# Optimization experiments

Hardware: AMD Instinct MI355X
Metric: run time of the kernel (lower is better)

Reference implementation:

```python
import jax, jax.numpy as jnp
import numpy as np

N_NODES, N_EDGES, B, K, D = 200000, 500000, 8192, 32, 128
E_DIM, E_EMB, N_CLASS = 128, 128, 60


def setup_inputs() -> dict:
    key = jax.random.key(0)
    ks = jax.random.split(key, 16)
    s = lambda k, shape, scale=0.05: jax.random.normal(k, shape, dtype=jnp.float32) * scale
    return {
        'memory_emb': s(ks[0], (N_NODES, D), 1.0),
        'edge_feat': s(ks[1], (N_EDGES, E_DIM), 1.0),
        'W_q': s(ks[2], (D, D)),
        'W_k': s(ks[3], (D, D)),
        'a': s(ks[4], (2 * D,)),
        'We_w': s(ks[5], (E_DIM, E_EMB)),
        'We_b': s(ks[6], (E_EMB,)),
        'Wuc': s(ks[7], (D + 2 * D + E_EMB, D)),
        'Wc1': s(ks[8], (D, 128)),
        'Wc2': s(ks[9], (128, N_CLASS)),
        'src_idxs': jax.random.randint(ks[10], (B,), 0, N_NODES),
        'dst_idxs': jax.random.randint(ks[11], (B,), 0, N_NODES),
        'edge_idxs': jax.random.randint(ks[12], (B,), 0, N_EDGES),
        'src_neighbors': jax.random.randint(ks[13], (B, K), 0, N_NODES),
        'dst_neighbors': jax.random.randint(ks[14], (B, K), 0, N_NODES),
    }


def reference(memory_emb, edge_feat, W_q, W_k, a, We_w, We_b, Wuc, Wc1, Wc2,
              src_idxs, dst_idxs, edge_idxs, src_neighbors, dst_neighbors):
    def attend(idxs, nbrs):
        self_emb = memory_emb[idxs]                      # [B, D] gather
        nb = memory_emb[nbrs]                            # [B, K, D] gather
        q = self_emb @ W_q                               # [B, D]
        k = jnp.einsum('bkd,de->bke', nb, W_k)           # [B, K, D]
        # GAT-style score: leaky_relu(a . [q || k])
        sq = q @ a[:D]                                   # [B]
        sk = jnp.einsum('bkd,d->bk', k, a[D:])           # [B, K]
        score = jax.nn.leaky_relu(sq[:, None] + sk, 0.2)
        attn = jax.nn.softmax(score, axis=-1)            # [B, K]
        agg = jnp.einsum('bk,bkd->bd', attn, k)          # [B, D]
        return self_emb, agg

    src_e, src_h = attend(src_idxs, src_neighbors)
    dst_e, dst_h = attend(dst_idxs, dst_neighbors)
    e = edge_feat[edge_idxs] @ We_w + We_b               # edge embedding [B, E_EMB]
    msg_src = jax.nn.relu(jnp.concatenate([src_e, src_h, dst_h, e], -1) @ Wuc)
    msg_dst = jax.nn.relu(jnp.concatenate([dst_e, dst_h, src_h, e], -1) @ Wuc)
    logits_src = jax.nn.relu(msg_src @ Wc1) @ Wc2
    logits_dst = jax.nn.relu(msg_dst @ Wc1) @ Wc2
    return jnp.stack([logits_src, logits_dst])           # [2, B, N_CLASS]
```

## Files before the change

### kernel.cpp

```cpp
#include <hip/hip_runtime.h>

#define D 128
#define KNBR 32
#define BATCH 8192
#define NCLASS 60

__global__ __launch_bounds__(256) void k_prep(const float* __restrict__ Wq,
                                              const float* __restrict__ Wk,
                                              const float* __restrict__ a,
                                              float* __restrict__ wqa,
                                              float* __restrict__ wka) {
    int tid = threadIdx.x;
    int i = tid & 127;
    const float* W  = (tid < 128) ? Wq : Wk;
    const float* av = (tid < 128) ? a  : a + D;
    float s = 0.f;
    for (int j = 0; j < D; ++j) s += W[i * D + j] * av[j];
    if (tid < 128) wqa[i] = s; else wka[i] = s;
}

__global__ __launch_bounds__(256) void k_attend(
    const float* __restrict__ mem, const float* __restrict__ Wk,
    const float* __restrict__ wqa, const float* __restrict__ wka,
    const int* __restrict__ src_idxs, const int* __restrict__ dst_idxs,
    const int* __restrict__ src_nb, const int* __restrict__ dst_nb,
    float* __restrict__ selfbuf, float* __restrict__ hbuf)
{
    int b = blockIdx.x;
    int side = blockIdx.y;
    const int* idxs = side ? dst_idxs : src_idxs;
    const int* nbrs = side ? dst_nb  : src_nb;
    int tid = threadIdx.x;

    __shared__ float s_self[D];
    __shared__ float s_wqa[D];
    __shared__ float s_wka[D];
    __shared__ float s_nb[KNBR][D];
    __shared__ int   s_idx[KNBR];
    __shared__ float s_red[D];
    __shared__ float s_skp[KNBR][8];
    __shared__ float s_attn[KNBR];
    __shared__ float s_nbsum[D];
    __shared__ float s_part[2][D];

    int node = idxs[b];
    if (tid < D) { s_self[tid] = mem[(size_t)node * D + tid]; s_wqa[tid] = wqa[tid]; }
    else         { s_wka[tid - D] = wka[tid - D]; }
    if (tid < KNBR) s_idx[tid] = nbrs[b * KNBR + tid];
    __syncthreads();

    {
        int row = tid >> 7;
        int col = tid & 127;
        for (int r = 0; r < KNBR; r += 2) {
            int nn = s_idx[r + row];
            s_nb[r + row][col] = mem[(size_t)nn * D + col];
        }
    }
    if (tid < D) s_red[tid] = s_self[tid] * s_wqa[tid];
    __syncthreads();
    for (int s = 64; s > 0; s >>= 1) {
        if (tid < s) s_red[tid] += s_red[tid + s];
        __syncthreads();
    }
    {
        int k = tid >> 3;
        int p = tid & 7;
        float acc = 0.f;
        int c0 = p * 16;
        #pragma unroll
        for (int c = 0; c < 16; ++c) acc += s_nb[k][c0 + c] * s_wka[c0 + c];
        s_skp[k][p] = acc;
    }
    __syncthreads();
    if (tid < KNBR) {
        float sk = 0.f;
        #pragma unroll
        for (int p = 0; p < 8; ++p) sk += s_skp[tid][p];
        float x = s_red[0] + sk;
        s_attn[tid] = (x >= 0.f) ? x : 0.2f * x;
    }
    __syncthreads();
    if (tid == 0) {
        float m = s_attn[0];
        for (int k = 1; k < KNBR; ++k) m = fmaxf(m, s_attn[k]);
        float sum = 0.f;
        for (int k = 0; k < KNBR; ++k) { float e = expf(s_attn[k] - m); s_attn[k] = e; sum += e; }
        float inv = 1.f / sum;
        for (int k = 0; k < KNBR; ++k) s_attn[k] *= inv;
    }
    __syncthreads();
    if (tid < D) {
        float acc = 0.f;
        #pragma unroll
        for (int k = 0; k < KNBR; ++k) acc += s_attn[k] * s_nb[k][tid];
        s_nbsum[tid] = acc;
    }
    __syncthreads();
    {
        int j = tid & 127;
        int half = tid >> 7;
        float acc = 0.f;
        for (int i = half * 64; i < half * 64 + 64; ++i)
            acc += s_nbsum[i] * Wk[i * D + j];
        s_part[half][j] = acc;
    }
    __syncthreads();
    size_t base = ((size_t)side * BATCH + b) * D;
    if (tid < D) {
        selfbuf[base + tid] = s_self[tid];
        hbuf[base + tid]    = s_part[0][tid] + s_part[1][tid];
    }
}

__global__ __launch_bounds__(256) void k_edge(
    const float* __restrict__ edge_feat, const float* __restrict__ Wew,
    const float* __restrict__ Web, const int* __restrict__ edge_idxs,
    float* __restrict__ ebuf)
{
    int b0 = blockIdx.x * 4;
    int tid = threadIdx.x;
    __shared__ float s_e[4][D];
    __shared__ float s_part[2][4][D];
    {
        int c = tid >> 7;
        int col = tid & 127;
        for (int cc = c; cc < 4; cc += 2) {
            int eidx = edge_idxs[b0 + cc];
            s_e[cc][col] = edge_feat[(size_t)eidx * D + col];
        }
    }
    __syncthreads();
    int j = tid & 127, half = tid >> 7;
    float a0 = 0, a1 = 0, a2 = 0, a3 = 0;
    for (int ii = 0; ii < 64; ++ii) {
        int i = half * 64 + ii;
        float w = Wew[i * D + j];
        a0 += s_e[0][i] * w; a1 += s_e[1][i] * w;
        a2 += s_e[2][i] * w; a3 += s_e[3][i] * w;
    }
    s_part[half][0][j] = a0; s_part[half][1][j] = a1;
    s_part[half][2][j] = a2; s_part[half][3][j] = a3;
    __syncthreads();
    if (tid < D) {
        float bias = Web[tid];
        #pragma unroll
        for (int c = 0; c < 4; ++c)
            ebuf[(size_t)(b0 + c) * D + tid] = s_part[0][c][tid] + s_part[1][c][tid] + bias;
    }
}

__global__ __launch_bounds__(256) void k_msg(
    const float* __restrict__ selfbuf, const float* __restrict__ hbuf,
    const float* __restrict__ ebuf, const float* __restrict__ Wuc,
    float* __restrict__ msgbuf)
{
    int side = blockIdx.y;
    int b0 = blockIdx.x * 8;
    int tid = threadIdx.x;
    __shared__ float s_cat[8][512];
    __shared__ float s_part[2][8][D];
    for (int t = tid; t < 8 * 512; t += 256) {
        int c = t >> 9;
        int i = t & 511;
        int bb = b0 + c;
        float v;
        if (i < 128)      v = selfbuf[((size_t)side * BATCH + bb) * D + i];
        else if (i < 256) v = hbuf[((size_t)side * BATCH + bb) * D + (i - 128)];
        else if (i < 384) v = hbuf[((size_t)(1 - side) * BATCH + bb) * D + (i - 256)];
        else              v = ebuf[(size_t)bb * D + (i - 384)];
        s_cat[c][i] = v;
    }
    __syncthreads();
    int j = tid & 127, half = tid >> 7;
    float acc[8] = {0, 0, 0, 0, 0, 0, 0, 0};
    for (int ii = 0; ii < 256; ++ii) {
        int i = half * 256 + ii;
        float w = Wuc[i * D + j];
        #pragma unroll
        for (int c = 0; c < 8; ++c) acc[c] += s_cat[c][i] * w;
    }
    #pragma unroll
    for (int c = 0; c < 8; ++c) s_part[half][c][j] = acc[c];
    __syncthreads();
    for (int t = tid; t < 8 * D; t += 256) {
        int c = t >> 7, j2 = t & 127;
        float v = s_part[0][c][j2] + s_part[1][c][j2];
        msgbuf[((size_t)side * BATCH + (b0 + c)) * D + j2] = fmaxf(v, 0.f);
    }
}

__global__ __launch_bounds__(256) void k_cls(
    const float* __restrict__ msgbuf, const float* __restrict__ Wc1,
    const float* __restrict__ Wc2, float* __restrict__ out)
{
    int side = blockIdx.y;
    int b0 = blockIdx.x * 4;
    int tid = threadIdx.x;
    __shared__ float s_m[4][D];
    __shared__ float s_part[2][4][D];
    __shared__ float s_h1[4][D];
    for (int t = tid; t < 4 * D; t += 256) {
        int c = t >> 7, j = t & 127;
        s_m[c][j] = msgbuf[((size_t)side * BATCH + (b0 + c)) * D + j];
    }
    __syncthreads();
    int j = tid & 127, half = tid >> 7;
    float a0 = 0, a1 = 0, a2 = 0, a3 = 0;
    for (int ii = 0; ii < 64; ++ii) {
        int i = half * 64 + ii;
        float w = Wc1[i * D + j];
        a0 += s_m[0][i] * w; a1 += s_m[1][i] * w;
        a2 += s_m[2][i] * w; a3 += s_m[3][i] * w;
    }
    s_part[half][0][j] = a0; s_part[half][1][j] = a1;
    s_part[half][2][j] = a2; s_part[half][3][j] = a3;
    __syncthreads();
    for (int t = tid; t < 4 * D; t += 256) {
        int c = t >> 7, j2 = t & 127;
        s_h1[c][j2] = fmaxf(s_part[0][c][j2] + s_part[1][c][j2], 0.f);
    }
    __syncthreads();
    if (tid < 4 * NCLASS) {
        int c = tid / NCLASS, j2 = tid % NCLASS;
        float acc = 0.f;
        for (int i = 0; i < D; ++i) acc += s_h1[c][i] * Wc2[i * NCLASS + j2];
        out[((size_t)side * BATCH + (b0 + c)) * NCLASS + j2] = acc;
    }
}

extern "C" void kernel_launch(void* const* d_in, const int* in_sizes, int n_in,
                              void* d_out, int out_size, void* d_ws, size_t ws_size,
                              hipStream_t stream) {
    const float* mem       = (const float*)d_in[0];
    const float* edge_feat = (const float*)d_in[1];
    const float* Wq        = (const float*)d_in[2];
    const float* Wk        = (const float*)d_in[3];
    const float* a         = (const float*)d_in[4];
    const float* Wew       = (const float*)d_in[5];
    const float* Web       = (const float*)d_in[6];
    const float* Wuc       = (const float*)d_in[7];
    const float* Wc1       = (const float*)d_in[8];
    const float* Wc2       = (const float*)d_in[9];
    const int* src_idxs    = (const int*)d_in[10];
    const int* dst_idxs    = (const int*)d_in[11];
    const int* edge_idxs   = (const int*)d_in[12];
    const int* src_nb      = (const int*)d_in[13];
    const int* dst_nb      = (const int*)d_in[14];
    float* out = (float*)d_out;

    float* ws = (float*)d_ws;
    float* wqa     = ws;
    float* wka     = ws + 128;
    float* selfbuf = ws + 256;
    float* hbuf    = selfbuf + 2 * (size_t)BATCH * D;
    float* ebuf    = hbuf    + 2 * (size_t)BATCH * D;
    float* msgbuf  = ebuf    + (size_t)BATCH * D;

    k_prep<<<1, 256, 0, stream>>>(Wq, Wk, a, wqa, wka);
    k_attend<<<dim3(BATCH, 2), 256, 0, stream>>>(mem, Wk, wqa, wka,
                                                 src_idxs, dst_idxs, src_nb, dst_nb,
                                                 selfbuf, hbuf);
    k_edge<<<BATCH / 4, 256, 0, stream>>>(edge_feat, Wew, Web, edge_idxs, ebuf);
    k_msg<<<dim3(BATCH / 8, 2), 256, 0, stream>>>(selfbuf, hbuf, ebuf, Wuc, msgbuf);
    k_cls<<<dim3(BATCH / 4, 2), 256, 0, stream>>>(msgbuf, Wc1, Wc2, out);
}
```

Measured before the change: 540.6 us.

## Fold Wk and edge weights into Wuc, tile message and classifier GEMMs

```diff
diff --git a/kernel.cpp b/kernel.cpp
--- a/kernel.cpp
+++ b/kernel.cpp
@@ -5,188 +5,223 @@
 #define BATCH 8192
 #define NCLASS 60
 
-__global__ __launch_bounds__(256) void k_prep(const float* __restrict__ Wq,
-                                              const float* __restrict__ Wk,
-                                              const float* __restrict__ a,
-                                              float* __restrict__ wqa,
-                                              float* __restrict__ wka) {
-    int tid = threadIdx.x;
-    int i = tid & 127;
-    const float* W  = (tid < 128) ? Wq : Wk;
-    const float* av = (tid < 128) ? a  : a + D;
-    float s = 0.f;
-    for (int j = 0; j < D; ++j) s += W[i * D + j] * av[j];
-    if (tid < 128) wqa[i] = s; else wka[i] = s;
+__global__ __launch_bounds__(256) void k_prep(
+    const float* __restrict__ Wq, const float* __restrict__ Wk,
+    const float* __restrict__ a, const float* __restrict__ Wew,
+    const float* __restrict__ Web, const float* __restrict__ Wuc,
+    float* __restrict__ wqa, float* __restrict__ wka,
+    float* __restrict__ be, float* __restrict__ Wcomb2)
+{
+    __shared__ float sB[128][129];
+    int blk = blockIdx.x, tid = threadIdx.x;
+    if (blk == 0) {
+        for (int t = tid; t < 128 * 128; t += 256) sB[t >> 7][t & 127] = Wq[t];
+        __syncthreads();
+        if (tid < 128) {
+            float s = 0.f;
+            for (int j = 0; j < D; ++j) s += sB[tid][j] * a[j];
+            wqa[tid] = s;
+        }
+        __syncthreads();
+        for (int t = tid; t < 128 * 128; t += 256) sB[t >> 7][t & 127] = Wk[t];
+        __syncthreads();
+        if (tid < 128) {
+            float s = 0.f;
+            for (int j = 0; j < D; ++j) s += sB[tid][j] * a[D + j];
+            wka[tid] = s;
+        }
+    } else if (blk == 1) {
+        if (tid < 128) {
+            float acc = 0.f;
+            for (int j = 0; j < D; ++j) acc += Web[j] * Wuc[(size_t)(384 + j) * D + tid];
+            be[tid] = acc;
+        }
+    } else {
+        int g  = (blk - 2) >> 4;
+        int rb = ((blk - 2) & 15) * 8;
+        const float* A = (g == 2) ? Wew : Wk;
+        const float* B = Wuc + (size_t)(128 + g * 128) * D;
+        for (int t = tid; t < 128 * 128; t += 256) sB[t >> 7][t & 127] = B[t];
+        __syncthreads();
+        int j = tid & 127, half = tid >> 7;
+        float acc[4] = {0.f, 0.f, 0.f, 0.f};
+        int r0 = rb + half * 4;
+        for (int t = 0; t < 128; ++t) {
+            float bv = sB[t][j];
+            #pragma unroll
+            for (int m = 0; m < 4; ++m)
+                acc[m] = fmaf(A[(size_t)(r0 + m) * D + t], bv, acc[m]);
+        }
+        #pragma unroll
+        for (int m = 0; m < 4; ++m)
+            Wcomb2[(size_t)(g * 128 + r0 + m) * D + j] = acc[m];
+    }
 }
 
 __global__ __launch_bounds__(256) void k_attend(
-    const float* __restrict__ mem, const float* __restrict__ Wk,
+    const float* __restrict__ mem,
     const float* __restrict__ wqa, const float* __restrict__ wka,
     const int* __restrict__ src_idxs, const int* __restrict__ dst_idxs,
     const int* __restrict__ src_nb, const int* __restrict__ dst_nb,
-    float* __restrict__ selfbuf, float* __restrict__ hbuf)
+    float* __restrict__ nbsumbuf)
 {
-    int b = blockIdx.x;
-    int side = blockIdx.y;
+    int b = blockIdx.x, side = blockIdx.y, tid = threadIdx.x;
     const int* idxs = side ? dst_idxs : src_idxs;
     const int* nbrs = side ? dst_nb  : src_nb;
-    int tid = threadIdx.x;
-
-    __shared__ float s_self[D];
-    __shared__ float s_wqa[D];
-    __shared__ float s_wka[D];
+
+    __shared__ int   s_idx[KNBR];
     __shared__ float s_nb[KNBR][D];
-    __shared__ int   s_idx[KNBR];
-    __shared__ float s_red[D];
-    __shared__ float s_skp[KNBR][8];
+    __shared__ float s_sk[KNBR];
     __shared__ float s_attn[KNBR];
-    __shared__ float s_nbsum[D];
+    __shared__ float s_sq;
     __shared__ float s_part[2][D];
 
-    int node = idxs[b];
-    if (tid < D) { s_self[tid] = mem[(size_t)node * D + tid]; s_wqa[tid] = wqa[tid]; }
-    else         { s_wka[tid - D] = wka[tid - D]; }
     if (tid < KNBR) s_idx[tid] = nbrs[b * KNBR + tid];
-    __syncthreads();
-
-    {
-        int row = tid >> 7;
-        int col = tid & 127;
-        for (int r = 0; r < KNBR; r += 2) {
-            int nn = s_idx[r + row];
-            s_nb[r + row][col] = mem[(size_t)nn * D + col];
-        }
-    }
-    if (tid < D) s_red[tid] = s_self[tid] * s_wqa[tid];
-    __syncthreads();
-    for (int s = 64; s > 0; s >>= 1) {
-        if (tid < s) s_red[tid] += s_red[tid + s];
-        __syncthreads();
-    }
-    {
-        int k = tid >> 3;
-        int p = tid & 7;
-        float acc = 0.f;
-        int c0 = p * 16;
-        #pragma unroll
-        for (int c = 0; c < 16; ++c) acc += s_nb[k][c0 + c] * s_wka[c0 + c];
-        s_skp[k][p] = acc;
-    }
-    __syncthreads();
-    if (tid < KNBR) {
-        float sk = 0.f;
-        #pragma unroll
-        for (int p = 0; p < 8; ++p) sk += s_skp[tid][p];
-        float x = s_red[0] + sk;
-        s_attn[tid] = (x >= 0.f) ? x : 0.2f * x;
-    }
-    __syncthreads();
-    if (tid == 0) {
-        float m = s_attn[0];
-        for (int k = 1; k < KNBR; ++k) m = fmaxf(m, s_attn[k]);
-        float sum = 0.f;
-        for (int k = 0; k < KNBR; ++k) { float e = expf(s_attn[k] - m); s_attn[k] = e; sum += e; }
-        float inv = 1.f / sum;
-        for (int k = 0; k < KNBR; ++k) s_attn[k] *= inv;
-    }
-    __syncthreads();
-    if (tid < D) {
-        float acc = 0.f;
-        #pragma unroll
-        for (int k = 0; k < KNBR; ++k) acc += s_attn[k] * s_nb[k][tid];
-        s_nbsum[tid] = acc;
-    }
-    __syncthreads();
-    {
-        int j = tid & 127;
-        int half = tid >> 7;
-        float acc = 0.f;
-        for (int i = half * 64; i < half * 64 + 64; ++i)
-            acc += s_nbsum[i] * Wk[i * D + j];
-        s_part[half][j] = acc;
-    }
-    __syncthreads();
-    size_t base = ((size_t)side * BATCH + b) * D;
-    if (tid < D) {
-        selfbuf[base + tid] = s_self[tid];
-        hbuf[base + tid]    = s_part[0][tid] + s_part[1][tid];
-    }
-}
-
-__global__ __launch_bounds__(256) void k_edge(
-    const float* __restrict__ edge_feat, const float* __restrict__ Wew,
-    const float* __restrict__ Web, const int* __restrict__ edge_idxs,
-    float* __restrict__ ebuf)
-{
-    int b0 = blockIdx.x * 4;
-    int tid = threadIdx.x;
-    __shared__ float s_e[4][D];
-    __shared__ float s_part[2][4][D];
-    {
-        int c = tid >> 7;
-        int col = tid & 127;
-        for (int cc = c; cc < 4; cc += 2) {
-            int eidx = edge_idxs[b0 + cc];
-            s_e[cc][col] = edge_feat[(size_t)eidx * D + col];
-        }
-    }
-    __syncthreads();
-    int j = tid & 127, half = tid >> 7;
-    float a0 = 0, a1 = 0, a2 = 0, a3 = 0;
-    for (int ii = 0; ii < 64; ++ii) {
-        int i = half * 64 + ii;
-        float w = Wew[i * D + j];
-        a0 += s_e[0][i] * w; a1 += s_e[1][i] * w;
-        a2 += s_e[2][i] * w; a3 += s_e[3][i] * w;
-    }
-    s_part[half][0][j] = a0; s_part[half][1][j] = a1;
-    s_part[half][2][j] = a2; s_part[half][3][j] = a3;
-    __syncthreads();
-    if (tid < D) {
-        float bias = Web[tid];
-        #pragma unroll
-        for (int c = 0; c < 4; ++c)
-            ebuf[(size_t)(b0 + c) * D + tid] = s_part[0][c][tid] + s_part[1][c][tid] + bias;
-    }
+    if (tid < 32) {
+        int node = idxs[b];
+        float4 self4 = ((const float4*)(mem + (size_t)node * D))[tid];
+        float4 wq4   = ((const float4*)wqa)[tid];
+        float p = self4.x * wq4.x + self4.y * wq4.y + self4.z * wq4.z + self4.w * wq4.w;
+        #pragma unroll
+        for (int m = 1; m <= 16; m <<= 1) p += __shfl_xor(p, m, 32);
+        if (tid == 0) s_sq = p;
+    }
+    __syncthreads();
+
+    int c4 = tid & 31;
+    int rbase = tid >> 5;
+    float4 wk4 = ((const float4*)wka)[c4];
+    #pragma unroll
+    for (int p = 0; p < 4; ++p) {
+        int r = rbase + 8 * p;
+        float4 v = ((const float4*)(mem + (size_t)s_idx[r] * D))[c4];
+        *(float4*)&s_nb[r][c4 * 4] = v;
+        float pr = v.x * wk4.x + v.y * wk4.y + v.z * wk4.z + v.w * wk4.w;
+        #pragma unroll
+        for (int m = 1; m <= 16; m <<= 1) pr += __shfl_xor(pr, m, 32);
+        if (c4 == 0) s_sk[r] = pr;
+    }
+    __syncthreads();
+
+    if (tid < 32) {
+        float x = s_sq + s_sk[tid];
+        x = (x >= 0.f) ? x : 0.2f * x;
+        float mx = x;
+        #pragma unroll
+        for (int m = 1; m <= 16; m <<= 1) mx = fmaxf(mx, __shfl_xor(mx, m, 32));
+        float e = __expf(x - mx);
+        float sum = e;
+        #pragma unroll
+        for (int m = 1; m <= 16; m <<= 1) sum += __shfl_xor(sum, m, 32);
+        s_attn[tid] = e / sum;
+    }
+    __syncthreads();
+
+    int col = tid & 127, half = tid >> 7;
+    float acc = 0.f;
+    int k0 = half * 16;
+    #pragma unroll
+    for (int k = 0; k < 16; ++k) acc = fmaf(s_attn[k0 + k], s_nb[k0 + k][col], acc);
+    s_part[half][col] = acc;
+    __syncthreads();
+    if (tid < 128)
+        nbsumbuf[((size_t)side * BATCH + b) * D + tid] = s_part[0][tid] + s_part[1][tid];
 }
 
 __global__ __launch_bounds__(256) void k_msg(
-    const float* __restrict__ selfbuf, const float* __restrict__ hbuf,
-    const float* __restrict__ ebuf, const float* __restrict__ Wuc,
-    float* __restrict__ msgbuf)
+    const float* __restrict__ mem, const float* __restrict__ edge_feat,
+    const float* __restrict__ Wuc, const float* __restrict__ Wcomb2,
+    const float* __restrict__ be,
+    const int* __restrict__ src_idxs, const int* __restrict__ dst_idxs,
+    const int* __restrict__ edge_idxs,
+    const float* __restrict__ nbsumbuf, float* __restrict__ msgbuf)
 {
     int side = blockIdx.y;
-    int b0 = blockIdx.x * 8;
+    int b0 = blockIdx.x * 64;
     int tid = threadIdx.x;
-    __shared__ float s_cat[8][512];
-    __shared__ float s_part[2][8][D];
-    for (int t = tid; t < 8 * 512; t += 256) {
-        int c = t >> 9;
-        int i = t & 511;
-        int bb = b0 + c;
-        float v;
-        if (i < 128)      v = selfbuf[((size_t)side * BATCH + bb) * D + i];
-        else if (i < 256) v = hbuf[((size_t)side * BATCH + bb) * D + (i - 128)];
-        else if (i < 384) v = hbuf[((size_t)(1 - side) * BATCH + bb) * D + (i - 256)];
-        else              v = ebuf[(size_t)bb * D + (i - 384)];
-        s_cat[c][i] = v;
-    }
-    __syncthreads();
-    int j = tid & 127, half = tid >> 7;
-    float acc[8] = {0, 0, 0, 0, 0, 0, 0, 0};
-    for (int ii = 0; ii < 256; ++ii) {
-        int i = half * 256 + ii;
-        float w = Wuc[i * D + j];
-        #pragma unroll
-        for (int c = 0; c < 8; ++c) acc[c] += s_cat[c][i] * w;
-    }
-    #pragma unroll
-    for (int c = 0; c < 8; ++c) s_part[half][c][j] = acc[c];
-    __syncthreads();
-    for (int t = tid; t < 8 * D; t += 256) {
-        int c = t >> 7, j2 = t & 127;
-        float v = s_part[0][c][j2] + s_part[1][c][j2];
-        msgbuf[((size_t)side * BATCH + (b0 + c)) * D + j2] = fmaxf(v, 0.f);
+
+    __shared__ float Ast[32][68];
+    __shared__ float Ws[32][128];
+    __shared__ int s_bidx[64], s_eidx[64];
+
+    if (tid < 64) {
+        s_bidx[tid] = (side ? dst_idxs : src_idxs)[b0 + tid];
+        s_eidx[tid] = edge_idxs[b0 + tid];
+    }
+    __syncthreads();
+
+    int tr = tid >> 4, tc = tid & 15;
+    int lc = tid & 31, lr = tid >> 5;
+    int wc = tid & 127, wk2 = tid >> 7;
+    float acc[4][8];
+    #pragma unroll
+    for (int i = 0; i < 4; ++i)
+        #pragma unroll
+        for (int j = 0; j < 8; ++j) acc[i][j] = 0.f;
+
+    for (int kt = 0; kt < 16; ++kt) {
+        int seg = kt >> 2, off = (kt & 3) * 32;
+        if (seg == 0) {
+            #pragma unroll
+            for (int p = 0; p < 8; ++p) {
+                int r = lr + 8 * p;
+                Ast[lc][r] = mem[(size_t)s_bidx[r] * D + off + lc];
+            }
+        } else if (seg == 1) {
+            #pragma unroll
+            for (int p = 0; p < 8; ++p) {
+                int r = lr + 8 * p;
+                Ast[lc][r] = nbsumbuf[((size_t)side * BATCH + b0 + r) * D + off + lc];
+            }
+        } else if (seg == 2) {
+            #pragma unroll
+            for (int p = 0; p < 8; ++p) {
+                int r = lr + 8 * p;
+                Ast[lc][r] = nbsumbuf[((size_t)(1 - side) * BATCH + b0 + r) * D + off + lc];
+            }
+        } else {
+            #pragma unroll
+            for (int p = 0; p < 8; ++p) {
+                int r = lr + 8 * p;
+                Ast[lc][r] = edge_feat[(size_t)s_eidx[r] * D + off + lc];
+            }
+        }
+        int krow0 = kt * 32;
+        #pragma unroll
+        for (int p = 0; p < 16; ++p) {
+            int kk = wk2 + 2 * p;
+            int gr = krow0 + kk;
+            Ws[kk][wc] = (gr < 128) ? Wuc[(size_t)gr * D + wc]
+                                    : Wcomb2[(size_t)(gr - 128) * D + wc];
+        }
+        __syncthreads();
+        #pragma unroll 4
+        for (int kk = 0; kk < 32; ++kk) {
+            float4 a4 = *(const float4*)&Ast[kk][tr * 4];
+            float4 w0 = *(const float4*)&Ws[kk][tc * 4];
+            float4 w1 = *(const float4*)&Ws[kk][64 + tc * 4];
+            float ar[4] = {a4.x, a4.y, a4.z, a4.w};
+            float wr[8] = {w0.x, w0.y, w0.z, w0.w, w1.x, w1.y, w1.z, w1.w};
+            #pragma unroll
+            for (int i = 0; i < 4; ++i)
+                #pragma unroll
+                for (int j = 0; j < 8; ++j)
+                    acc[i][j] = fmaf(ar[i], wr[j], acc[i][j]);
+        }
+        __syncthreads();
+    }
+
+    float4 bv0 = *(const float4*)&be[tc * 4];
+    float4 bv1 = *(const float4*)&be[64 + tc * 4];
+    #pragma unroll
+    for (int i = 0; i < 4; ++i) {
+        size_t row = (size_t)side * BATCH + b0 + tr * 4 + i;
+        float4 o0 = make_float4(fmaxf(acc[i][0] + bv0.x, 0.f), fmaxf(acc[i][1] + bv0.y, 0.f),
+                                fmaxf(acc[i][2] + bv0.z, 0.f), fmaxf(acc[i][3] + bv0.w, 0.f));
+        float4 o1 = make_float4(fmaxf(acc[i][4] + bv1.x, 0.f), fmaxf(acc[i][5] + bv1.y, 0.f),
+                                fmaxf(acc[i][6] + bv1.z, 0.f), fmaxf(acc[i][7] + bv1.w, 0.f));
+        *(float4*)&msgbuf[row * D + tc * 4] = o0;
+        *(float4*)&msgbuf[row * D + 64 + tc * 4] = o1;
     }
 }
 
@@ -195,37 +230,93 @@
     const float* __restrict__ Wc2, float* __restrict__ out)
 {
     int side = blockIdx.y;
-    int b0 = blockIdx.x * 4;
+    int b0 = blockIdx.x * 32;
     int tid = threadIdx.x;
-    __shared__ float s_m[4][D];
-    __shared__ float s_part[2][4][D];
-    __shared__ float s_h1[4][D];
-    for (int t = tid; t < 4 * D; t += 256) {
-        int c = t >> 7, j = t & 127;
-        s_m[c][j] = msgbuf[((size_t)side * BATCH + (b0 + c)) * D + j];
-    }
-    __syncthreads();
-    int j = tid & 127, half = tid >> 7;
-    float a0 = 0, a1 = 0, a2 = 0, a3 = 0;
-    for (int ii = 0; ii < 64; ++ii) {
-        int i = half * 64 + ii;
-        float w = Wc1[i * D + j];
-        a0 += s_m[0][i] * w; a1 += s_m[1][i] * w;
-        a2 += s_m[2][i] * w; a3 += s_m[3][i] * w;
-    }
-    s_part[half][0][j] = a0; s_part[half][1][j] = a1;
-    s_part[half][2][j] = a2; s_part[half][3][j] = a3;
-    __syncthreads();
-    for (int t = tid; t < 4 * D; t += 256) {
-        int c = t >> 7, j2 = t & 127;
-        s_h1[c][j2] = fmaxf(s_part[0][c][j2] + s_part[1][c][j2], 0.f);
-    }
-    __syncthreads();
-    if (tid < 4 * NCLASS) {
-        int c = tid / NCLASS, j2 = tid % NCLASS;
-        float acc = 0.f;
-        for (int i = 0; i < D; ++i) acc += s_h1[c][i] * Wc2[i * NCLASS + j2];
-        out[((size_t)side * BATCH + (b0 + c)) * NCLASS + j2] = acc;
+
+    __shared__ float Ast[32][36];
+    __shared__ float Ws[32][128];
+    __shared__ float HsT[128][36];
+    __shared__ float Wc2s[128][64];
+
+    for (int t = tid; t < 128 * 60; t += 256) {
+        int kk = t / 60, c = t - kk * 60;
+        Wc2s[kk][c] = Wc2[t];
+    }
+
+    int tr = tid >> 4, tc = tid & 15;
+    int lc = tid & 31, lr = tid >> 5;
+    int wc = tid & 127, wk2 = tid >> 7;
+    float acc[2][8];
+    #pragma unroll
+    for (int i = 0; i < 2; ++i)
+        #pragma unroll
+        for (int j = 0; j < 8; ++j) acc[i][j] = 0.f;
+
+    for (int kt = 0; kt < 4; ++kt) {
+        int off = kt * 32;
+        #pragma unroll
+        for (int p = 0; p < 4; ++p) {
+            int r = lr + 8 * p;
+            Ast[lc][r] = msgbuf[((size_t)side * BATCH + b0 + r) * D + off + lc];
+        }
+        #pragma unroll
+        for (int p = 0; p < 16; ++p) {
+            int kk = wk2 + 2 * p;
+            Ws[kk][wc] = Wc1[(size_t)(off + kk) * D + wc];
+        }
+        __syncthreads();
+        #pragma unroll 4
+        for (int kk = 0; kk < 32; ++kk) {
+            float2 a2 = *(const float2*)&Ast[kk][tr * 2];
+            float4 w0 = *(const float4*)&Ws[kk][tc * 4];
+            float4 w1 = *(const float4*)&Ws[kk][64 + tc * 4];
+            float ar[2] = {a2.x, a2.y};
+            float wr[8] = {w0.x, w0.y, w0.z, w0.w, w1.x, w1.y, w1.z, w1.w};
+            #pragma unroll
+            for (int i = 0; i < 2; ++i)
+                #pragma unroll
+                for (int j = 0; j < 8; ++j)
+                    acc[i][j] = fmaf(ar[i], wr[j], acc[i][j]);
+        }
+        __syncthreads();
+    }
+
+    #pragma unroll
+    for (int i = 0; i < 2; ++i) {
+        int r = tr * 2 + i;
+        #pragma unroll
+        for (int j = 0; j < 4; ++j) {
+            HsT[tc * 4 + j][r]      = fmaxf(acc[i][j], 0.f);
+            HsT[64 + tc * 4 + j][r] = fmaxf(acc[i][j + 4], 0.f);
+        }
+    }
+    __syncthreads();
+
+    int r0 = (tid >> 4) * 2;
+    int cg = tid & 15;
+    int c0 = cg * 4;
+    float acc2[2][4];
+    #pragma unroll
+    for (int i = 0; i < 2; ++i)
+        #pragma unroll
+        for (int j = 0; j < 4; ++j) acc2[i][j] = 0.f;
+    for (int kk = 0; kk < 128; ++kk) {
+        float2 h2 = *(const float2*)&HsT[kk][r0];
+        float4 w4 = *(const float4*)&Wc2s[kk][c0];
+        float wr[4] = {w4.x, w4.y, w4.z, w4.w};
+        #pragma unroll
+        for (int j = 0; j < 4; ++j) {
+            acc2[0][j] = fmaf(h2.x, wr[j], acc2[0][j]);
+            acc2[1][j] = fmaf(h2.y, wr[j], acc2[1][j]);
+        }
+    }
+    if (cg < 15) {
+        #pragma unroll
+        for (int i = 0; i < 2; ++i) {
+            size_t row = (size_t)side * BATCH + b0 + r0 + i;
+            *(float4*)&out[row * NCLASS + c0] =
+                make_float4(acc2[i][0], acc2[i][1], acc2[i][2], acc2[i][3]);
+        }
     }
 }
 
@@ -250,18 +341,19 @@
     float* out = (float*)d_out;
 
     float* ws = (float*)d_ws;
-    float* wqa     = ws;
-    float* wka     = ws + 128;
-    float* selfbuf = ws + 256;
-    float* hbuf    = selfbuf + 2 * (size_t)BATCH * D;
-    float* ebuf    = hbuf    + 2 * (size_t)BATCH * D;
-    float* msgbuf  = ebuf    + (size_t)BATCH * D;
-
-    k_prep<<<1, 256, 0, stream>>>(Wq, Wk, a, wqa, wka);
-    k_attend<<<dim3(BATCH, 2), 256, 0, stream>>>(mem, Wk, wqa, wka,
+    float* Wcomb2 = ws;
+    float* be     = ws + 49152;
+    float* wqa    = ws + 49280;
+    float* wka    = ws + 49408;
+    float* nbsum  = ws + 49536;
+    float* msgbuf = nbsum + 2097152;
+
+    k_prep<<<50, 256, 0, stream>>>(Wq, Wk, a, Wew, Web, Wuc, wqa, wka, be, Wcomb2);
+    k_attend<<<dim3(BATCH, 2), 256, 0, stream>>>(mem, wqa, wka,
                                                  src_idxs, dst_idxs, src_nb, dst_nb,
-                                                 selfbuf, hbuf);
-    k_edge<<<BATCH / 4, 256, 0, stream>>>(edge_feat, Wew, Web, edge_idxs, ebuf);
-    k_msg<<<dim3(BATCH / 8, 2), 256, 0, stream>>>(selfbuf, hbuf, ebuf, Wuc, msgbuf);
-    k_cls<<<dim3(BATCH / 4, 2), 256, 0, stream>>>(msgbuf, Wc1, Wc2, out);
-}
+                                                 nbsum);
+    k_msg<<<dim3(BATCH / 64, 2), 256, 0, stream>>>(mem, edge_feat, Wuc, Wcomb2, be,
+                                                   src_idxs, dst_idxs, edge_idxs,
+                                                   nbsum, msgbuf);
+    k_cls<<<dim3(BATCH / 32, 2), 256, 0, stream>>>(msgbuf, Wc1, Wc2, out);
+}
```

New measurement: 541.8 us. About the same (+0.2%).
